# Performance work log

Measured on AMD Instinct MI355X. Metric: run time of the kernel, lower is better.

The kernel has to match this reference:

```python
import jax, jax.numpy as jnp
import numpy as np

EPS = 1e-5

def _ternary(w):
    # BitNet 1.58-bit: per-output-channel scale = median(|W|) (scale_op='median'),
    # quantize to {-1,0,1}*scale with straight-through estimator.
    s = jnp.maximum(jnp.median(jnp.abs(w), axis=(1, 2, 3), keepdims=True), EPS)
    q = jnp.clip(jnp.round(w / s), -1.0, 1.0) * s
    return w + jax.lax.stop_gradient(q - w)

def _conv3x3(x, w):
    # NCHW, OIHW, stride 1, pad 1 (spatial-preserving)
    return jax.lax.conv_general_dilated(
        x, _ternary(w), (1, 1), ((1, 1), (1, 1)),
        dimension_numbers=('NCHW', 'OIHW', 'NCHW'))

def _bn(y, g, b, m, v):
    # eval-mode BatchNorm2d folded to a single scale/shift
    inv = g / jnp.sqrt(v + EPS)
    return y * inv[None, :, None, None] + (b - m * inv)[None, :, None, None]

def _ssh(x, p):
    (w3, g3, b3, m3, v3,
     ws, gs, bs, ms, vs,
     w5, g5, b5, m5, v5,
     w7a, g7a, b7a, m7a, v7a,
     w7b, g7b, b7b, m7b, v7b) = p
    c3 = _bn(_conv3x3(x, w3), g3, b3, m3, v3)                      # [B, half, H, W]
    stem = jax.nn.silu(_bn(_conv3x3(x, ws), gs, bs, ms, vs))       # [B, quart, H, W]
    c5 = _bn(_conv3x3(stem, w5), g5, b5, m5, v5)                   # [B, quart, H, W]
    t = jax.nn.silu(_bn(_conv3x3(stem, w7a), g7a, b7a, m7a, v7a))
    c7 = _bn(_conv3x3(t, w7b), g7b, b7b, m7b, v7b)                 # [B, quart, H, W]
    return jax.nn.silu(jnp.concatenate((c3, c5, c7), axis=1))      # [B, out_ch, H, W]

def setup_inputs() -> dict:
    key = jax.random.key(0)
    B, CIN, H, W = 32, 256, 64, 64
    HALF, Q = 128, 64  # out_ch=256 -> half=128, quart=64
    d = {"x": jax.random.normal(jax.random.fold_in(key, 0), (B, CIN, H, W), jnp.float32)}

    def mk(i, o, c):
        k0, k1, k2, k3, k4 = jax.random.split(jax.random.fold_in(key, i), 5)
        return (jax.random.normal(k0, (o, c, 3, 3), jnp.float32) * 0.05,
                1.0 + 0.1 * jax.random.normal(k1, (o,), jnp.float32),   # gamma
                0.1 * jax.random.normal(k2, (o,), jnp.float32),          # beta
                0.1 * jax.random.normal(k3, (o,), jnp.float32),          # running mean
                0.5 + jax.random.uniform(k4, (o,), jnp.float32))         # running var > 0

    for name, (o, c), i in [("3", (HALF, CIN), 1), ("s", (Q, CIN), 2),
                            ("5", (Q, Q), 3), ("7a", (Q, Q), 4), ("7b", (Q, Q), 5)]:
        w, g, b, m, v = mk(i, o, c)
        d["w" + name] = w; d["g" + name] = g; d["b" + name] = b
        d["m" + name] = m; d["v" + name] = v
    return d

def reference(x,
              w3, g3, b3, m3, v3,
              ws, gs, bs, ms, vs,
              w5, g5, b5, m5, v5,
              w7a, g7a, b7a, m7a, v7a,
              w7b, g7b, b7b, m7b, v7b):
    return _ssh(x, (w3, g3, b3, m3, v3, ws, gs, bs, ms, vs,
                    w5, g5, b5, m5, v5, w7a, g7a, b7a, m7a, v7a,
                    w7b, g7b, b7b, m7b, v7b))
```

## Files before the change

kernel.cpp:

```cpp
#include <hip/hip_runtime.h>
#include <stdint.h>

#define EPSF 1e-5f

typedef __bf16 bf16;
typedef __attribute__((ext_vector_type(8))) __bf16 bf16x8;
typedef __attribute__((ext_vector_type(4))) float f32x4;

#define GL16(src, dst) __builtin_amdgcn_global_load_lds( \
    (const __attribute__((address_space(1))) void*)(src), \
    (__attribute__((address_space(3))) void*)(dst), 16, 0, 0)
#define MEMFENCE() asm volatile("" ::: "memory")

struct QArgs {
  const float* w[5];
  const float* g[5];
  const float* bb[5];
  const float* m[5];
  const float* v[5];
  bf16* wpk[3];
  float* alpha[3];
  float* beta[3];
};

__global__ __launch_bounds__(256)
void quant_kernel(QArgs qa) {
  __shared__ int red[2][4];
  const int tid = threadIdx.x;
  const int blk = blockIdx.x;
  int layer, o;
  if (blk < 128)      { layer = 0; o = blk; }
  else if (blk < 192) { layer = 1; o = blk - 128; }
  else if (blk < 256) { layer = 2; o = blk - 192; }
  else if (blk < 320) { layer = 3; o = blk - 256; }
  else                { layer = 4; o = blk - 320; }
  const int I_[5]     = {256, 256, 64, 64, 64};
  const int gemm_[5]  = {0, 0, 1, 1, 2};
  const int obase_[5] = {0, 128, 0, 64, 0};
  const int gNMT[3]   = {12, 8, 4};
  const int I = I_[layer];
  const int n = I * 9;
  const float* w = qa.w[layer] + (size_t)o * n;

  unsigned key[9];
#pragma unroll
  for (int j = 0; j < 9; ++j) key[j] = 0xFFFFFFFFu;
  {
    int c2 = 0;
    for (int i = tid; i < n; i += 256) key[c2++] = __float_as_uint(fabsf(w[i]));
  }

  const int wv = tid >> 6;
  unsigned pfx[2] = {0u, 0u};
  const int rank0 = n / 2 - 1, rank1 = n / 2;
  int pp = 0;
  for (int bit = 31; bit >= 0; --bit) {
    const unsigned c0 = pfx[0] | (1u << bit);
    const unsigned c1 = pfx[1] | (1u << bit);
    int loc = 0;
#pragma unroll
    for (int j = 0; j < 9; ++j)
      loc += (key[j] < c0 ? 1 : 0) + (key[j] < c1 ? 0x10000 : 0);
    loc += __shfl_xor(loc, 32); loc += __shfl_xor(loc, 16);
    loc += __shfl_xor(loc, 8);  loc += __shfl_xor(loc, 4);
    loc += __shfl_xor(loc, 2);  loc += __shfl_xor(loc, 1);
    if ((tid & 63) == 0) red[pp][wv] = loc;
    __syncthreads();
    const int tot = red[pp][0] + red[pp][1] + red[pp][2] + red[pp][3];
    if ((tot & 0xFFFF) <= rank0) pfx[0] = c0;
    if ((tot >> 16)    <= rank1) pfx[1] = c1;
    pp ^= 1;
  }
  const float s =
      fmaxf(0.5f * (__uint_as_float(pfx[0]) + __uint_as_float(pfx[1])), EPSF);

  const int g  = gemm_[layer];
  const int ob = obase_[layer];
  const int NMT = gNMT[g];
  if (tid == 0) {
    float inv = qa.g[layer][o] / sqrtf(qa.v[layer][o] + EPSF);
    qa.alpha[g][ob + o] = s * inv;
    qa.beta[g][ob + o]  = qa.bb[layer][o] - qa.m[layer][o] * inv;
  }
  const int og  = ob + o;
  const int mt  = og >> 4;
  const int l16 = og & 15;
  bf16* wp = qa.wpk[g];
  for (int i = tid; i < n; i += 256) {
    float t = rintf(w[i] / s);
    t = fmaxf(-1.f, fminf(1.f, t));
    int c = i / 9, pos = i % 9;
    int k = pos * I + c;
    int ks = k >> 5, kq = (k >> 3) & 3, jj = k & 7;
    wp[((size_t)((ks * NMT + mt) * 64 + kq * 16 + l16)) * 8 + jj] = (bf16)t;
  }
}

__global__ __launch_bounds__(256)
void transpose_k(const float* __restrict__ x, bf16* __restrict__ xT,
                 float* __restrict__ zp) {
  if (blockIdx.x == 0 && threadIdx.x < 16) zp[threadIdx.x] = 0.0f;
  __shared__ float tile[64 * 66];
  const int tid = threadIdx.x;
  const int blk = blockIdx.x;
  const int cg = blk & 3;
  const int h  = (blk >> 2) & 63;
  const int b  = blk >> 8;
  const int w  = tid & 63;
  const int cb = tid >> 6;
#pragma unroll
  for (int p = 0; p < 16; ++p) {
    int c = cb * 16 + p;
    tile[w * 66 + c] = x[(((size_t)(b * 256 + cg * 64 + c)) * 64 + h) * 64 + w];
  }
  __syncthreads();
#pragma unroll
  for (int p = 0; p < 2; ++p) {
    int id = tid + p * 256;
    int c8 = id & 7, w2 = id >> 3;
    const float* src = &tile[w2 * 66 + c8 * 8];
    bf16x8 v;
#pragma unroll
    for (int j = 0; j < 8; ++j) v[j] = (bf16)src[j];
    *(bf16x8*)&xT[(((size_t)(b * 64 + h)) * 64 + w2) * 256 + cg * 64 + c8 * 8] = v;
  }
}

template<int CIN, int NMT, int MM, int C1, bool HASPAD>
__global__ __launch_bounds__(512, 4)
void conv_k(const bf16* __restrict__ xin,
            const bf16* __restrict__ wpk,
            const float* __restrict__ alpha,
            const float* __restrict__ beta,
            float* __restrict__ out, int chan_off,
            bf16* __restrict__ padout,
            const bf16* __restrict__ zpage) {
  constexpr int NC = CIN / 32;
  __shared__ __align__(16) union U {
    bf16 xs[2][8704];
    bf16 ep[128 * 72];
  } sm;

  const int tid  = threadIdx.x;
  const int wave = tid >> 6;
  const int lane = tid & 63;
  const int q    = lane >> 4;
  const int t16  = lane & 15;
  const int rw   = wave >> 2;
  const int mt0  = (wave & 3) * MM;
  const int b    = blockIdx.x >> 5;
  const int h0   = (blockIdx.x & 31) << 1;

  const bf16* srcp[3];
  int step[3];
#pragma unroll
  for (int p = 0; p < 3; ++p) {
    const int id = tid + p * 512;
    const int c8p = id & 3, rj = id >> 2;
    const int j = rj % 66, r = rj / 66;
    const int hh = h0 + r - 1, ww = j - 1;
    const bool v = (id < 1056) && ((unsigned)hh < 64u) && ((unsigned)ww < 64u);
    const int c8 = c8p ^ ((j >> 1) & 3);
    srcp[p] = v ? &xin[(((size_t)(b * 64 + hh)) * 64 + ww) * CIN + c8 * 8] : zpage;
    step[p] = v ? 32 : 0;
  }

  int Caddr[3];
#pragma unroll
  for (int kw = 0; kw < 3; ++kw) {
    const int col = t16 + kw;
    Caddr[kw] = rw * 4224 + col * 64 + ((q ^ ((col >> 1) & 3)) << 4);
  }

  char* const lds0 = (char*)&sm.xs[0][0];

  GL16(srcp[0], lds0 + wave * 1024);
  GL16(srcp[1], lds0 + 8192 + wave * 1024);
  if (wave == 0) GL16(srcp[2], lds0 + 16384);
  MEMFENCE();
#pragma unroll
  for (int p = 0; p < 3; ++p) srcp[p] += step[p];

  bf16x8 aE[MM], aO[MM];
#pragma unroll
  for (int mm = 0; mm < MM; ++mm)
    aE[mm] = *(const bf16x8*)&wpk[((size_t)(mt0 + mm) * 64 + lane) * 8];

  f32x4 acc[4][MM] = {};
  int tog = 17408;

  for (int ci = 0; ci < NC; ++ci) {
    if (ci == 0) {
      if constexpr (MM == 3) asm volatile("s_waitcnt vmcnt(3)" ::: "memory");
      else if constexpr (MM == 2) asm volatile("s_waitcnt vmcnt(2)" ::: "memory");
      else asm volatile("s_waitcnt vmcnt(1)" ::: "memory");
    } else {
      if constexpr (MM == 3) asm volatile("s_waitcnt vmcnt(27)" ::: "memory");
      else if constexpr (MM == 2) asm volatile("s_waitcnt vmcnt(18)" ::: "memory");
      else asm volatile("s_waitcnt vmcnt(9)" ::: "memory");
    }
    __builtin_amdgcn_s_barrier();
    if (ci + 1 < NC) {
      char* lb = lds0 + (((ci + 1) & 1) ? 17408 : 0);
      GL16(srcp[0], lb + wave * 1024);
      GL16(srcp[1], lb + 8192 + wave * 1024);
      if (wave == 0) GL16(srcp[2], lb + 16384);
#pragma unroll
      for (int p = 0; p < 3; ++p) srcp[p] += step[p];
    }
    MEMFENCE();
#pragma unroll
    for (int pos = 0; pos < 9; ++pos) {
      if (pos < 8) {
        const int ksn = (pos + 1) * NC + ci;
        bf16x8* an = ((pos + 1) & 1) ? aO : aE;
#pragma unroll
        for (int mm = 0; mm < MM; ++mm)
          an[mm] = *(const bf16x8*)&wpk[((size_t)(ksn * NMT + mt0 + mm) * 64 + lane) * 8];
      }
      const bf16x8* ac = (pos & 1) ? aO : aE;
      const int kh = pos / 3, kw = pos % 3;
#pragma unroll
      for (int nt = 0; nt < 4; ++nt) {
        const bf16x8 bv =
            *(const bf16x8*)(lds0 + (Caddr[kw] + nt * 1024 + kh * 4224));
#pragma unroll
        for (int mm = 0; mm < MM; ++mm)
          acc[nt][mm] = __builtin_amdgcn_mfma_f32_16x16x32_bf16(ac[mm], bv, acc[nt][mm], 0, 0, 0);
      }
      if (pos == 8 && ci + 1 < NC) {
#pragma unroll
        for (int mm = 0; mm < MM; ++mm)
          aE[mm] = *(const bf16x8*)&wpk[((size_t)((ci + 1) * NMT + mt0 + mm) * 64 + lane) * 8];
      }
    }
#pragma unroll
    for (int kw = 0; kw < 3; ++kw) Caddr[kw] += tog;
    tog = -tog;
  }

  const int h = h0 + rw;
#pragma unroll
  for (int mm = 0; mm < MM; ++mm) {
    const int o0 = (mt0 + mm) * 16 + 4 * q;
    float av[4], bv2[4];
#pragma unroll
    for (int i = 0; i < 4; ++i) { av[i] = alpha[o0 + i]; bv2[i] = beta[o0 + i]; }
#pragma unroll
    for (int nt = 0; nt < 4; ++nt) {
      const int wv = nt * 16 + t16;
#pragma unroll
      for (int i = 0; i < 4; ++i) {
        float v = acc[nt][mm][i] * av[i] + bv2[i];
        float sg = v / (1.f + __expf(-v));
        acc[nt][mm][i] = sg;
        if (o0 < C1)
          out[(((size_t)(b * 256 + chan_off + o0 + i)) * 64 + h) * 64 + wv] = sg;
      }
    }
  }
  if (HASPAD) {
    __syncthreads();
#pragma unroll
    for (int mm = 0; mm < MM; ++mm) {
      const int o0 = (mt0 + mm) * 16 + 4 * q;
      if (o0 >= C1) {
#pragma unroll
        for (int nt = 0; nt < 4; ++nt) {
          const int px = rw * 64 + nt * 16 + t16;
          union { bf16 h4[4]; uint2 u; } pk;
#pragma unroll
          for (int i = 0; i < 4; ++i) pk.h4[i] = (bf16)acc[nt][mm][i];
          *(uint2*)&sm.ep[px * 72 + (o0 - C1)] = pk.u;
        }
      }
    }
    __syncthreads();
#pragma unroll
    for (int p = 0; p < 2; ++p) {
      int id = tid + p * 512;
      int c8 = id & 7, px = id >> 3;
      bf16x8 v = *(const bf16x8*)&sm.ep[px * 72 + c8 * 8];
      const int r = px >> 6, wv2 = px & 63;
      *(bf16x8*)&padout[(((size_t)(b * 64 + h0 + r)) * 64 + wv2) * 64 + c8 * 8] = v;
    }
  }
}

extern "C" void kernel_launch(void* const* d_in, const int* in_sizes, int n_in,
                              void* d_out, int out_size, void* d_ws, size_t ws_size,
                              hipStream_t stream) {
  QArgs qa;
  const float* x = (const float*)d_in[0];
  for (int L = 0; L < 5; ++L) {
    qa.w[L]  = (const float*)d_in[1 + 5 * L];
    qa.g[L]  = (const float*)d_in[2 + 5 * L];
    qa.bb[L] = (const float*)d_in[3 + 5 * L];
    qa.m[L]  = (const float*)d_in[4 + 5 * L];
    qa.v[L]  = (const float*)d_in[5 + 5 * L];
  }
  char* p = (char*)d_ws;
  bf16* wpk1 = (bf16*)p; p += (size_t)192 * 2304 * 2;
  bf16* wpk2 = (bf16*)p; p += (size_t)128 * 576 * 2;
  bf16* wpk3 = (bf16*)p; p += (size_t)64 * 576 * 2;
  float* a1 = (float*)p; p += 1024;
  float* b1 = (float*)p; p += 1024;
  float* a2 = (float*)p; p += 1024;
  float* b2 = (float*)p; p += 1024;
  float* a3 = (float*)p; p += 1024;
  float* b3 = (float*)p; p += 1024;
  float* zp = (float*)p; p += 64;
  bf16* xT   = (bf16*)p; p += (size_t)32 * 64 * 64 * 256 * 2;
  bf16* stem = (bf16*)p; p += (size_t)32 * 64 * 64 * 64 * 2;
  bf16* tbuf = xT;
  qa.wpk[0] = wpk1; qa.wpk[1] = wpk2; qa.wpk[2] = wpk3;
  qa.alpha[0] = a1; qa.alpha[1] = a2; qa.alpha[2] = a3;
  qa.beta[0]  = b1; qa.beta[1]  = b2; qa.beta[2]  = b3;

  quant_kernel<<<384, 256, 0, stream>>>(qa);
  transpose_k<<<32 * 64 * 4, 256, 0, stream>>>(x, xT, zp);

  const bf16* zpb = (const bf16*)zp;
  conv_k<256, 12, 3, 128, true ><<<1024, 512, 0, stream>>>(xT,   wpk1, a1, b1, (float*)d_out, 0,   stem, zpb);
  conv_k< 64,  8, 2,  64, true ><<<1024, 512, 0, stream>>>(stem, wpk2, a2, b2, (float*)d_out, 128, tbuf, zpb);
  conv_k< 64,  4, 1,  64, false><<<1024, 512, 0, stream>>>(tbuf, wpk3, a3, b3, (float*)d_out, 192, nullptr, zpb);
}
```

Baseline: 453.0 us.

## Deepen weight-fragment prefetch, preload both chunks for small convs, vectorize transpose

The conv kernel now uses a three-deep rotating register buffer for weight fragments, prefetching two positions ahead instead of one, and tightens the vmcnt wait accordingly. For the 64-channel convs (two K chunks), both input chunks are loaded into LDS up front, which removes the per-chunk barrier and reload. MFMA sections run at raised wave priority via s_setprio. The transpose kernel reads x with float4 loads and reads LDS with float2, and the zero page is enlarged. The cost is extra register pressure from the third fragment buffer, and the hand-counted vmcnt values must exactly match the number of outstanding loads.

```diff
diff --git a/kernel.cpp b/kernel.cpp
--- a/kernel.cpp
+++ b/kernel.cpp
@@ -11,6 +11,13 @@
     (const __attribute__((address_space(1))) void*)(src), \
     (__attribute__((address_space(3))) void*)(dst), 16, 0, 0)
 #define MEMFENCE() asm volatile("" ::: "memory")
+
+template<int N> __device__ __forceinline__ void vwait() {
+  static_assert(N == 2 || N == 4 || N == 6, "unsupported vmcnt");
+  if constexpr (N == 2) asm volatile("s_waitcnt vmcnt(2)" ::: "memory");
+  else if constexpr (N == 4) asm volatile("s_waitcnt vmcnt(4)" ::: "memory");
+  else asm volatile("s_waitcnt vmcnt(6)" ::: "memory");
+}
 
 struct QArgs {
   const float* w[5];
@@ -99,19 +106,24 @@
 __global__ __launch_bounds__(256)
 void transpose_k(const float* __restrict__ x, bf16* __restrict__ xT,
                  float* __restrict__ zp) {
-  if (blockIdx.x == 0 && threadIdx.x < 16) zp[threadIdx.x] = 0.0f;
+  if (blockIdx.x == 0 && threadIdx.x < 32) zp[threadIdx.x] = 0.0f;
   __shared__ float tile[64 * 66];
   const int tid = threadIdx.x;
   const int blk = blockIdx.x;
   const int cg = blk & 3;
   const int h  = (blk >> 2) & 63;
   const int b  = blk >> 8;
-  const int w  = tid & 63;
-  const int cb = tid >> 6;
-#pragma unroll
-  for (int p = 0; p < 16; ++p) {
-    int c = cb * 16 + p;
-    tile[w * 66 + c] = x[(((size_t)(b * 256 + cg * 64 + c)) * 64 + h) * 64 + w];
+  const int w4 = (tid & 15) * 4;
+  const int cb = tid >> 4;
+#pragma unroll
+  for (int p = 0; p < 4; ++p) {
+    int c = cb + p * 16;
+    const float4 v =
+        *(const float4*)&x[(((size_t)(b * 256 + cg * 64 + c)) * 64 + h) * 64 + w4];
+    tile[(w4 + 0) * 66 + c] = v.x;
+    tile[(w4 + 1) * 66 + c] = v.y;
+    tile[(w4 + 2) * 66 + c] = v.z;
+    tile[(w4 + 3) * 66 + c] = v.w;
   }
   __syncthreads();
 #pragma unroll
@@ -119,9 +131,13 @@
     int id = tid + p * 256;
     int c8 = id & 7, w2 = id >> 3;
     const float* src = &tile[w2 * 66 + c8 * 8];
+    float2 f0 = *(const float2*)(src + 0);
+    float2 f1 = *(const float2*)(src + 2);
+    float2 f2 = *(const float2*)(src + 4);
+    float2 f3 = *(const float2*)(src + 6);
     bf16x8 v;
-#pragma unroll
-    for (int j = 0; j < 8; ++j) v[j] = (bf16)src[j];
+    v[0] = (bf16)f0.x; v[1] = (bf16)f0.y; v[2] = (bf16)f1.x; v[3] = (bf16)f1.y;
+    v[4] = (bf16)f2.x; v[5] = (bf16)f2.y; v[6] = (bf16)f3.x; v[7] = (bf16)f3.y;
     *(bf16x8*)&xT[(((size_t)(b * 64 + h)) * 64 + w2) * 256 + cg * 64 + c8 * 8] = v;
   }
 }
@@ -177,48 +193,57 @@
   GL16(srcp[0], lds0 + wave * 1024);
   GL16(srcp[1], lds0 + 8192 + wave * 1024);
   if (wave == 0) GL16(srcp[2], lds0 + 16384);
+  if constexpr (NC == 2) {
+    GL16(srcp[0] + step[0], lds0 + 17408 + wave * 1024);
+    GL16(srcp[1] + step[1], lds0 + 17408 + 8192 + wave * 1024);
+    if (wave == 0) GL16(srcp[2] + step[2], lds0 + 17408 + 16384);
+  } else {
+#pragma unroll
+    for (int p = 0; p < 3; ++p) srcp[p] += step[p];
+  }
   MEMFENCE();
-#pragma unroll
-  for (int p = 0; p < 3; ++p) srcp[p] += step[p];
-
-  bf16x8 aE[MM], aO[MM];
-#pragma unroll
-  for (int mm = 0; mm < MM; ++mm)
-    aE[mm] = *(const bf16x8*)&wpk[((size_t)(mt0 + mm) * 64 + lane) * 8];
+
+  bf16x8 fr[3][MM];
+#pragma unroll
+  for (int mm = 0; mm < MM; ++mm) {
+    fr[0][mm] = *(const bf16x8*)&wpk[((size_t)(mt0 + mm) * 64 + lane) * 8];
+    fr[1][mm] = *(const bf16x8*)&wpk[((size_t)(NC * NMT + mt0 + mm) * 64 + lane) * 8];
+  }
 
   f32x4 acc[4][MM] = {};
   int tog = 17408;
 
   for (int ci = 0; ci < NC; ++ci) {
-    if (ci == 0) {
-      if constexpr (MM == 3) asm volatile("s_waitcnt vmcnt(3)" ::: "memory");
-      else if constexpr (MM == 2) asm volatile("s_waitcnt vmcnt(2)" ::: "memory");
-      else asm volatile("s_waitcnt vmcnt(1)" ::: "memory");
-    } else {
-      if constexpr (MM == 3) asm volatile("s_waitcnt vmcnt(27)" ::: "memory");
-      else if constexpr (MM == 2) asm volatile("s_waitcnt vmcnt(18)" ::: "memory");
-      else asm volatile("s_waitcnt vmcnt(9)" ::: "memory");
-    }
-    __builtin_amdgcn_s_barrier();
-    if (ci + 1 < NC) {
-      char* lb = lds0 + (((ci + 1) & 1) ? 17408 : 0);
-      GL16(srcp[0], lb + wave * 1024);
-      GL16(srcp[1], lb + 8192 + wave * 1024);
-      if (wave == 0) GL16(srcp[2], lb + 16384);
-#pragma unroll
-      for (int p = 0; p < 3; ++p) srcp[p] += step[p];
+    if (NC > 2 || ci == 0) {
+      vwait<2 * MM>();
+      __builtin_amdgcn_s_barrier();
+    }
+    if constexpr (NC > 2) {
+      if (ci + 1 < NC) {
+        char* lb = lds0 + (((ci + 1) & 1) ? 17408 : 0);
+        GL16(srcp[0], lb + wave * 1024);
+        GL16(srcp[1], lb + 8192 + wave * 1024);
+        if (wave == 0) GL16(srcp[2], lb + 16384);
+#pragma unroll
+        for (int p = 0; p < 3; ++p) srcp[p] += step[p];
+      }
     }
     MEMFENCE();
+    __builtin_amdgcn_s_setprio(1);
 #pragma unroll
     for (int pos = 0; pos < 9; ++pos) {
-      if (pos < 8) {
-        const int ksn = (pos + 1) * NC + ci;
-        bf16x8* an = ((pos + 1) & 1) ? aO : aE;
+      const int t = pos + 2;
+      if (t <= 8) {
+        const int ksn = t * NC + ci;
 #pragma unroll
         for (int mm = 0; mm < MM; ++mm)
-          an[mm] = *(const bf16x8*)&wpk[((size_t)(ksn * NMT + mt0 + mm) * 64 + lane) * 8];
-      }
-      const bf16x8* ac = (pos & 1) ? aO : aE;
+          fr[t % 3][mm] = *(const bf16x8*)&wpk[((size_t)(ksn * NMT + mt0 + mm) * 64 + lane) * 8];
+      } else if (ci + 1 < NC) {
+        const int ksn = (t - 9) * NC + (ci + 1);
+#pragma unroll
+        for (int mm = 0; mm < MM; ++mm)
+          fr[t % 3][mm] = *(const bf16x8*)&wpk[((size_t)(ksn * NMT + mt0 + mm) * 64 + lane) * 8];
+      }
       const int kh = pos / 3, kw = pos % 3;
 #pragma unroll
       for (int nt = 0; nt < 4; ++nt) {
@@ -226,14 +251,10 @@
             *(const bf16x8*)(lds0 + (Caddr[kw] + nt * 1024 + kh * 4224));
 #pragma unroll
         for (int mm = 0; mm < MM; ++mm)
-          acc[nt][mm] = __builtin_amdgcn_mfma_f32_16x16x32_bf16(ac[mm], bv, acc[nt][mm], 0, 0, 0);
-      }
-      if (pos == 8 && ci + 1 < NC) {
-#pragma unroll
-        for (int mm = 0; mm < MM; ++mm)
-          aE[mm] = *(const bf16x8*)&wpk[((size_t)((ci + 1) * NMT + mt0 + mm) * 64 + lane) * 8];
-      }
-    }
+          acc[nt][mm] = __builtin_amdgcn_mfma_f32_16x16x32_bf16(fr[pos % 3][mm], bv, acc[nt][mm], 0, 0, 0);
+      }
+    }
+    __builtin_amdgcn_s_setprio(0);
 #pragma unroll
     for (int kw = 0; kw < 3; ++kw) Caddr[kw] += tog;
     tog = -tog;
@@ -309,7 +330,7 @@
   float* b2 = (float*)p; p += 1024;
   float* a3 = (float*)p; p += 1024;
   float* b3 = (float*)p; p += 1024;
-  float* zp = (float*)p; p += 64;
+  float* zp = (float*)p; p += 128;
   bf16* xT   = (bf16*)p; p += (size_t)32 * 64 * 64 * 256 * 2;
   bf16* stem = (bf16*)p; p += (size_t)32 * 64 * 64 * 64 * 2;
   bf16* tbuf = xT;
```

Measured after the change: 434.4 us. -4.1%, faster.
